# Kernel tuning notes

Hardware: AMD Instinct MI355X
Metric: run time of the kernel (lower is better)

The kernel has to match this reference:

```python
import jax, jax.numpy as jnp
import numpy as np

B, N, C = 8192, 4, 4096
SINKHORN_ITERS = 3
EPS = 1e-6


def setup_inputs() -> dict:
    key = jax.random.key(0)
    k1, k2, k3, k4 = jax.random.split(key, 4)
    x = jax.random.normal(k1, (B, N, C), dtype=jnp.float32)
    rmsnorm_weight = jnp.ones((C,), dtype=jnp.float32)  # init: ones (bf16 param, used as float)
    H_pre = jax.random.normal(k2, (N,), dtype=jnp.float32) * 0.1   # init zeros; small noise for testing
    H_post = jax.random.normal(k3, (N,), dtype=jnp.float32) * 0.1
    H_res = jnp.eye(N, dtype=jnp.float32) + 0.1 * jax.random.normal(k4, (N, N), dtype=jnp.float32)
    return {"x": x, "rmsnorm_weight": rmsnorm_weight, "H_pre": H_pre, "H_post": H_post, "H_res": H_res}


def _sinkhorn(P, iters, eps):
    # 4x4 matrix: alternate row / column normalization
    for _ in range(iters):
        P = P / (P.sum(axis=-1, keepdims=True) + eps)
        P = P / (P.sum(axis=-2, keepdims=True) + eps)
    return P


def reference(x, rmsnorm_weight, H_pre, H_post, H_res):
    x32 = x.astype(jnp.float32)                       # [B, n, C]
    H_pre_act = jax.nn.sigmoid(H_pre)                 # [n]
    # weighted aggregation over the n streams: matmul(x^T, sigmoid(H_pre))
    x_agg = jnp.einsum('bnc,n->bc', x32, H_pre_act)   # [B, C]
    # RMSNorm (computed in fp32, output cast to bf16, matching the fallback path)
    rms = jnp.sqrt(jnp.mean(x_agg * x_agg, axis=-1, keepdims=True) + EPS)
    y_norm = ((x_agg / rms) * rmsnorm_weight).astype(jnp.bfloat16)  # [B, C]
    # Sinkhorn-normalized 4x4 mixing matrix
    M = _sinkhorn(jnp.exp(H_res), SINKHORN_ITERS, EPS)  # [n, n]
    H_post_act = 2.0 * jax.nn.sigmoid(H_post)           # [n]
    # bmm with M broadcast over batch
    mixed = jnp.einsum('nm,bmc->bnc', M, x32)           # [B, n, C]
    out = mixed + H_post_act[None, :, None] * y_norm.astype(jnp.float32)[:, None, :]
    return out
```

## Files before the change

### kernel.cpp

```cpp
#include <hip/hip_runtime.h>
#include <hip/hip_bf16.h>
#include <math.h>


constexpr float kEPS = 1e-6f;

__global__ void mhc_prep(const float* __restrict__ H_pre,
                         const float* __restrict__ H_post,
                         const float* __restrict__ H_res,
                         float* __restrict__ ws) {
  if (threadIdx.x != 0 || blockIdx.x != 0) return;
  float P[4][4];
  #pragma unroll
  for (int i = 0; i < 4; ++i)
    #pragma unroll
    for (int j = 0; j < 4; ++j)
      P[i][j] = expf(H_res[i * 4 + j]);
  for (int it = 0; it < 3; ++it) {
    #pragma unroll
    for (int i = 0; i < 4; ++i) {
      float s = P[i][0] + P[i][1] + P[i][2] + P[i][3] + kEPS;
      float r = 1.0f / s;
      #pragma unroll
      for (int j = 0; j < 4; ++j) P[i][j] *= r;
    }
    #pragma unroll
    for (int j = 0; j < 4; ++j) {
      float s = P[0][j] + P[1][j] + P[2][j] + P[3][j] + kEPS;
      float r = 1.0f / s;
      #pragma unroll
      for (int i = 0; i < 4; ++i) P[i][j] *= r;
    }
  }
  #pragma unroll
  for (int n = 0; n < 4; ++n) ws[n] = 1.0f / (1.0f + expf(-H_pre[n]));
  #pragma unroll
  for (int n = 0; n < 4; ++n) ws[4 + n] = 2.0f / (1.0f + expf(-H_post[n]));
  #pragma unroll
  for (int i = 0; i < 4; ++i)
    #pragma unroll
    for (int j = 0; j < 4; ++j)
      ws[8 + i * 4 + j] = P[i][j];
}

__device__ __forceinline__ float uni(float v) {
  return __int_as_float(__builtin_amdgcn_readfirstlane(__float_as_int(v)));
}

__device__ __forceinline__ float bf16_round(float v) {
  unsigned u = __float_as_uint(v);
  u = (u + 0x7fffu + ((u >> 16) & 1u)) & 0xffff0000u;
  return __uint_as_float(u);
}

__global__ __launch_bounds__(256) void mhc_main(
    const float4* __restrict__ x4,
    const float4* __restrict__ w4,
    const float* __restrict__ ws,
    float4* __restrict__ out4) {
  const int b = blockIdx.x;
  const int tid = threadIdx.x;

  float hpre[4], hpost[4], M[4][4];
  #pragma unroll
  for (int n = 0; n < 4; ++n) hpre[n] = uni(ws[n]);
  #pragma unroll
  for (int n = 0; n < 4; ++n) hpost[n] = uni(ws[4 + n]);
  #pragma unroll
  for (int i = 0; i < 4; ++i)
    #pragma unroll
    for (int j = 0; j < 4; ++j)
      M[i][j] = uni(ws[8 + i * 4 + j]);

  const size_t rowBase = (size_t)b * 4096;

  float xv[4][16];
  #pragma unroll
  for (int n = 0; n < 4; ++n) {
    #pragma unroll
    for (int k = 0; k < 4; ++k) {
      float4 t = x4[rowBase + n * 1024 + k * 256 + tid];
      xv[n][k * 4 + 0] = t.x; xv[n][k * 4 + 1] = t.y;
      xv[n][k * 4 + 2] = t.z; xv[n][k * 4 + 3] = t.w;
    }
  }

  float agg[16];
  #pragma unroll
  for (int j = 0; j < 16; ++j)
    agg[j] = hpre[0] * xv[0][j] + hpre[1] * xv[1][j] +
             hpre[2] * xv[2][j] + hpre[3] * xv[3][j];

  float ssq = 0.0f;
  #pragma unroll
  for (int j = 0; j < 16; ++j) ssq += agg[j] * agg[j];
  #pragma unroll
  for (int off = 32; off > 0; off >>= 1) ssq += __shfl_xor(ssq, off, 64);

  __shared__ float sred[4];
  const int wave = tid >> 6;
  const int lane = tid & 63;
  if (lane == 0) sred[wave] = ssq;
  __syncthreads();
  const float total = sred[0] + sred[1] + sred[2] + sred[3];
  const float inv = 1.0f / sqrtf(total * (1.0f / 4096.0f) + kEPS);

  float yn[16];
  #pragma unroll
  for (int k = 0; k < 4; ++k) {
    float4 t = w4[k * 256 + tid];
    yn[k * 4 + 0] = bf16_round(agg[k * 4 + 0] * inv * t.x);
    yn[k * 4 + 1] = bf16_round(agg[k * 4 + 1] * inv * t.y);
    yn[k * 4 + 2] = bf16_round(agg[k * 4 + 2] * inv * t.z);
    yn[k * 4 + 3] = bf16_round(agg[k * 4 + 3] * inv * t.w);
  }

  #pragma unroll
  for (int n = 0; n < 4; ++n) {
    #pragma unroll
    for (int k = 0; k < 4; ++k) {
      float4 o;
      #pragma unroll
      for (int c = 0; c < 4; ++c) {
        const int j = k * 4 + c;
        float v = M[n][0] * xv[0][j] + M[n][1] * xv[1][j] +
                  M[n][2] * xv[2][j] + M[n][3] * xv[3][j] +
                  hpost[n] * yn[j];
        (&o.x)[c] = v;
      }
      out4[rowBase + n * 1024 + k * 256 + tid] = o;
    }
  }
}

extern "C" void kernel_launch(void* const* d_in, const int* in_sizes, int n_in,
                              void* d_out, int out_size, void* d_ws, size_t ws_size,
                              hipStream_t stream) {
  const float* x      = (const float*)d_in[0];
  const float* w      = (const float*)d_in[1];
  const float* H_pre  = (const float*)d_in[2];
  const float* H_post = (const float*)d_in[3];
  const float* H_res  = (const float*)d_in[4];
  float* out = (float*)d_out;
  float* ws  = (float*)d_ws;

  mhc_prep<<<1, 64, 0, stream>>>(H_pre, H_post, H_res, ws);
  mhc_main<<<8192, 256, 0, stream>>>((const float4*)x, (const float4*)w, ws,
                                     (float4*)out);
}
```

Before: 208.9 us.

## Use 1024-thread blocks with one float4 per stream and nontemporal loads/stores

Each block now runs 1024 threads, so every thread handles one float4 per stream instead of four, which cuts per-thread register use and raises the number of resident waves. Loads of x and stores of out use nontemporal hints to avoid polluting the cache with streaming data, and x loads are issued before the workspace reads. The cross-wave reduction now sums 16 partials, and the larger blocks may make block scheduling less flexible.

```diff
diff --git a/kernel.cpp b/kernel.cpp
--- a/kernel.cpp
+++ b/kernel.cpp
@@ -4,6 +4,8 @@
 
 
 constexpr float kEPS = 1e-6f;
+
+typedef float f32x4 __attribute__((ext_vector_type(4)));
 
 __global__ void mhc_prep(const float* __restrict__ H_pre,
                          const float* __restrict__ H_post,
@@ -53,13 +55,20 @@
   return __uint_as_float(u);
 }
 
-__global__ __launch_bounds__(256) void mhc_main(
-    const float4* __restrict__ x4,
-    const float4* __restrict__ w4,
+__global__ __launch_bounds__(1024) void mhc_main(
+    const f32x4* __restrict__ x4,
+    const f32x4* __restrict__ w4,
     const float* __restrict__ ws,
-    float4* __restrict__ out4) {
+    f32x4* __restrict__ out4) {
   const int b = blockIdx.x;
   const int tid = threadIdx.x;
+  const size_t rowBase = (size_t)b * 4096;
+
+  f32x4 xv[4];
+  #pragma unroll
+  for (int n = 0; n < 4; ++n)
+    xv[n] = __builtin_nontemporal_load(&x4[rowBase + n * 1024 + tid]);
+  const f32x4 wv = w4[tid];
 
   float hpre[4], hpost[4], M[4][4];
   #pragma unroll
@@ -72,64 +81,32 @@
     for (int j = 0; j < 4; ++j)
       M[i][j] = uni(ws[8 + i * 4 + j]);
 
-  const size_t rowBase = (size_t)b * 4096;
+  f32x4 agg = hpre[0] * xv[0] + hpre[1] * xv[1] + hpre[2] * xv[2] + hpre[3] * xv[3];
 
-  float xv[4][16];
-  #pragma unroll
-  for (int n = 0; n < 4; ++n) {
-    #pragma unroll
-    for (int k = 0; k < 4; ++k) {
-      float4 t = x4[rowBase + n * 1024 + k * 256 + tid];
-      xv[n][k * 4 + 0] = t.x; xv[n][k * 4 + 1] = t.y;
-      xv[n][k * 4 + 2] = t.z; xv[n][k * 4 + 3] = t.w;
-    }
-  }
-
-  float agg[16];
-  #pragma unroll
-  for (int j = 0; j < 16; ++j)
-    agg[j] = hpre[0] * xv[0][j] + hpre[1] * xv[1][j] +
-             hpre[2] * xv[2][j] + hpre[3] * xv[3][j];
-
-  float ssq = 0.0f;
-  #pragma unroll
-  for (int j = 0; j < 16; ++j) ssq += agg[j] * agg[j];
+  float ssq = agg.x * agg.x + agg.y * agg.y + agg.z * agg.z + agg.w * agg.w;
   #pragma unroll
   for (int off = 32; off > 0; off >>= 1) ssq += __shfl_xor(ssq, off, 64);
 
-  __shared__ float sred[4];
+  __shared__ float sred[16];
   const int wave = tid >> 6;
   const int lane = tid & 63;
   if (lane == 0) sred[wave] = ssq;
   __syncthreads();
-  const float total = sred[0] + sred[1] + sred[2] + sred[3];
+  float total = 0.0f;
+  #pragma unroll
+  for (int i = 0; i < 16; ++i) total += sred[i];
   const float inv = 1.0f / sqrtf(total * (1.0f / 4096.0f) + kEPS);
 
-  float yn[16];
+  f32x4 yn;
   #pragma unroll
-  for (int k = 0; k < 4; ++k) {
-    float4 t = w4[k * 256 + tid];
-    yn[k * 4 + 0] = bf16_round(agg[k * 4 + 0] * inv * t.x);
-    yn[k * 4 + 1] = bf16_round(agg[k * 4 + 1] * inv * t.y);
-    yn[k * 4 + 2] = bf16_round(agg[k * 4 + 2] * inv * t.z);
-    yn[k * 4 + 3] = bf16_round(agg[k * 4 + 3] * inv * t.w);
-  }
+  for (int c = 0; c < 4; ++c)
+    yn[c] = bf16_round(agg[c] * inv * wv[c]);
 
   #pragma unroll
   for (int n = 0; n < 4; ++n) {
-    #pragma unroll
-    for (int k = 0; k < 4; ++k) {
-      float4 o;
-      #pragma unroll
-      for (int c = 0; c < 4; ++c) {
-        const int j = k * 4 + c;
-        float v = M[n][0] * xv[0][j] + M[n][1] * xv[1][j] +
-                  M[n][2] * xv[2][j] + M[n][3] * xv[3][j] +
-                  hpost[n] * yn[j];
-        (&o.x)[c] = v;
-      }
-      out4[rowBase + n * 1024 + k * 256 + tid] = o;
-    }
+    f32x4 o = M[n][0] * xv[0] + M[n][1] * xv[1] + M[n][2] * xv[2] +
+              M[n][3] * xv[3] + hpost[n] * yn;
+    __builtin_nontemporal_store(o, &out4[rowBase + n * 1024 + tid]);
   }
 }
 
@@ -145,6 +122,6 @@
   float* ws  = (float*)d_ws;
 
   mhc_prep<<<1, 64, 0, stream>>>(H_pre, H_post, H_res, ws);
-  mhc_main<<<8192, 256, 0, stream>>>((const float4*)x, (const float4*)w, ws,
-                                     (float4*)out);
+  mhc_main<<<8192, 1024, 0, stream>>>((const f32x4*)x, (const f32x4*)w, ws,
+                                      (f32x4*)out);
 }
```

Result: faster. 180.9 us (median of 2 runs) (-13.4%).
